# Kernel tuning notes

Hardware: AMD Instinct MI355X
Metric: run time of the kernel (lower is better)

The kernel has to match this reference:

```python
import jax, jax.numpy as jnp
import numpy as np

IMG_SIZE = 224
PATCH_SIZE = 16
CONTEXT_LEN = 316
LATENT_DIM = 1024
NUM_HEADS = 16
NUM_PATCHES = (IMG_SIZE // PATCH_SIZE) ** 2  # 196
SEQ_LEN = NUM_PATCHES + CONTEXT_LEN          # 512
BATCH = 8


def prefix_lm_mask(num_img_patches, total):
    # lower-triangular causal mask, but the image-patch block is fully bidirectional
    m = np.tril(np.ones((total, total), dtype=np.float32))
    m[:num_img_patches, :num_img_patches] = 1.0
    return jnp.asarray(m)  # [S, S], 1 = attend, 0 = masked


def setup_inputs() -> dict:
    key = jax.random.key(0)
    k_x, k_q, k_k, k_v, k_o, k_b = jax.random.split(key, 6)
    d = LATENT_DIM
    scale = 1.0 / np.sqrt(d)
    return {
        "x": jax.random.normal(k_x, (BATCH, SEQ_LEN, d), dtype=jnp.float32),
        "w_q": jax.random.normal(k_q, (d, d), dtype=jnp.float32) * scale,
        "w_k": jax.random.normal(k_k, (d, d), dtype=jnp.float32) * scale,
        "w_v": jax.random.normal(k_v, (d, d), dtype=jnp.float32) * scale,
        "w_o": jax.random.normal(k_o, (d, d), dtype=jnp.float32) * scale,
        "b_o": jax.random.normal(k_b, (d,), dtype=jnp.float32) * 0.01,
    }


def reference(x, w_q, w_k, w_v, w_o, b_o):
    B, S, D = x.shape
    H = NUM_HEADS
    hd = D // H
    # projections (nn.Linear: y = x @ W^T)
    q = (x @ w_q.T).reshape(B, S, H, hd).transpose(0, 2, 1, 3)  # [B,H,S,hd]
    k = (x @ w_k.T).reshape(B, S, H, hd).transpose(0, 2, 1, 3)
    v = (x @ w_v.T).reshape(B, S, H, hd).transpose(0, 2, 1, 3)
    scores = jnp.einsum("bhqd,bhkd->bhqk", q, k) / jnp.sqrt(jnp.float32(hd))
    mask = prefix_lm_mask(NUM_PATCHES, S)  # [S,S]
    scores = jnp.where(mask == 0, jnp.float32(-jnp.inf), scores)
    attn = jax.nn.softmax(scores, axis=-1)
    ctx = jnp.einsum("bhqk,bhkd->bhqd", attn, v)
    ctx = ctx.transpose(0, 2, 1, 3).reshape(B, S, D)
    return ctx @ w_o.T + b_o
```

## Files before the change

kernel.cpp:

```cpp
#include <hip/hip_runtime.h>
#include <stdint.h>
#include <math.h>

#define NB_B 8
#define NB_S 512
#define NB_D 1024
#define NB_H 16
#define NB_HD 64
#define NP 196
#define MTOT 4096

#define OFF_XB 0
#define OFF_WQ 4194304
#define OFF_WK 5242880
#define OFF_WV 6291456
#define OFF_WO 7340032
#define OFF_Q  8388608
#define OFF_K  12582912
#define OFF_VT 16777216
#define OFF_CT 20971520

typedef __attribute__((ext_vector_type(8))) short bf16x8;
typedef __attribute__((ext_vector_type(4))) float f32x4;
typedef __attribute__((ext_vector_type(4))) short s16x4;
typedef __attribute__((ext_vector_type(8))) short s16x8;

__device__ __forceinline__ short f2bf(float f) {
  union { float f; uint32_t u; } c; c.f = f;
  uint32_t r = (c.u + 0x7fffu + ((c.u >> 16) & 1u)) >> 16;
  return (short)r;
}

__device__ __forceinline__ uint32_t pack2bf(float lo, float hi) {
  uint32_t ulo = __float_as_uint(lo) + 0x8000u;
  uint32_t uhi = __float_as_uint(hi) + 0x8000u;
  return __builtin_amdgcn_perm(uhi, ulo, 0x07060302u);
}

__device__ __forceinline__ void async16(void* lds, const void* g) {
  __builtin_amdgcn_global_load_lds(
      (const __attribute__((address_space(1))) void*)g,
      (__attribute__((address_space(3))) void*)lds, 16, 0, 0);
}

__global__ __launch_bounds__(256) void cvt5(const float* __restrict__ x,
                                            const float* __restrict__ wq,
                                            const float* __restrict__ wk,
                                            const float* __restrict__ wv,
                                            const float* __restrict__ wo,
                                            short* __restrict__ ws) {
  __shared__ uint32_t lt[16 * 513];
  int b = blockIdx.x, t = threadIdx.x;
  const float* src; short* dst; float scale;
  if (b < 256) {
    src = x + b * 16384;
    dst = ws + OFF_XB + b * 16384;
    scale = 1.0f;
  } else {
    int wi = (b - 256) >> 6, gn = (b - 256) & 63;
    switch (wi) {
      case 0:  src = wq + gn * 16384; scale = 0.125f; break;
      case 1:  src = wk + gn * 16384; scale = 1.0f;   break;
      case 2:  src = wv + gn * 16384; scale = 1.0f;   break;
      default: src = wo + gn * 16384; scale = 1.0f;   break;
    }
    dst = ws + OFF_WQ + wi * 1048576 + gn * 16384;
  }
#pragma unroll
  for (int i = 0; i < 16; ++i) {
    int flat = t + i * 256;
    int row = flat >> 8, col4 = flat & 255;
    float4 v = *(const float4*)(src + flat * 4);
    uint32_t lo = (uint32_t)(uint16_t)f2bf(v.x * scale) |
                  ((uint32_t)(uint16_t)f2bf(v.y * scale) << 16);
    uint32_t hi = (uint32_t)(uint16_t)f2bf(v.z * scale) |
                  ((uint32_t)(uint16_t)f2bf(v.w * scale) << 16);
    lt[row * 513 + col4 * 2]     = lo;
    lt[row * 513 + col4 * 2 + 1] = hi;
  }
  __syncthreads();
#pragma unroll
  for (int i = 0; i < 8; ++i) {
    int s = t + i * 256;
    int kb = s >> 6, l = s & 63, quad = l >> 4, cc = l & 15;
    int base = cc * 513 + kb * 16 + quad * 4;
    union { uint32_t u[4]; s16x8 v; } o;
    o.u[0] = lt[base];     o.u[1] = lt[base + 1];
    o.u[2] = lt[base + 2]; o.u[3] = lt[base + 3];
    *(s16x8*)(dst + s * 8) = o.v;
  }
}

__global__ __launch_bounds__(256, 2) void gemm_qkv(short* __restrict__ ws) {
  __shared__ __align__(16) short As[4096];
  __shared__ __align__(16) short Bs[4096];
  int bx = blockIdx.x;
  int wsel = bx >> 8;
  int tile = bx & 255;
  int mt = tile >> 3, nt = tile & 7;
  int m0 = mt << 7, n0 = nt << 7;
  const short* A  = ws + OFF_XB;
  const short* Bw = ws + OFF_WQ + wsel * 1048576;
  int t = threadIdx.x, lane = t & 63, wvi = t >> 6;
  int c = lane & 15, quad = lane >> 4;
  int wm = wvi >> 1, wn = wvi & 1;
  int g0 = mt << 3, gn0 = nt << 3;
  f32x4 acc[4][4] = {};

  for (int kk = 0; kk < 1024; kk += 32) {
    int kb = kk >> 5;
#pragma unroll
    for (int i = 0; i < 2; ++i) {
      int ch = wvi * 2 + i;
      async16(&As[ch << 9], A  + ((g0  + ch) * 32 + kb) * 512 + lane * 8);
      async16(&Bs[ch << 9], Bw + ((gn0 + ch) * 32 + kb) * 512 + lane * 8);
    }
    __syncthreads();
    bf16x8 af[4], bfr[4];
#pragma unroll
    for (int i = 0; i < 4; ++i) af[i]  = *(const bf16x8*)&As[((wm * 4 + i) << 9) + lane * 8];
#pragma unroll
    for (int j = 0; j < 4; ++j) bfr[j] = *(const bf16x8*)&Bs[((wn * 4 + j) << 9) + lane * 8];
#pragma unroll
    for (int i = 0; i < 4; ++i)
#pragma unroll
      for (int j = 0; j < 4; ++j)
        acc[i][j] = __builtin_amdgcn_mfma_f32_16x16x32_bf16(af[i], bfr[j], acc[i][j], 0, 0, 0);
    __syncthreads();
  }

#pragma unroll
  for (int i = 0; i < 4; ++i) {
#pragma unroll
    for (int j = 0; j < 4; ++j) {
      int n = n0 + wn * 64 + j * 16 + c;
      int h = n >> 6, d = n & 63;
      int mq = m0 + wm * 64 + i * 16 + quad * 4;
      int bb = mq >> 9, srow = mq & 511;
      if (wsel < 2) {
        int dblk = d >> 5, qk = (d >> 3) & 3, jd = d & 7;
        int g = srow >> 4;
        short* outp = ws + (wsel == 0 ? OFF_Q : OFF_K);
        size_t base = (size_t)(bb * 16 + h) * 32768 +
                      (size_t)(((g * 2 + dblk) * 64 + qk * 16 + quad * 4)) * 8 + jd;
#pragma unroll
        for (int r = 0; r < 4; ++r) outp[base + r * 8] = f2bf(acc[i][j][r]);
      } else {
        int dg = d >> 4, cv = d & 15;
        int kblk = srow >> 5, qv = (srow >> 3) & 3, jv = srow & 7;
        s16x4 o;
#pragma unroll
        for (int r = 0; r < 4; ++r) o[r] = f2bf(acc[i][j][r]);
        *(s16x4*)&ws[OFF_VT + (size_t)(bb * 16 + h) * 32768 +
                     (size_t)((dg * 16 + kblk) * 64 + qv * 16 + cv) * 8 + jv] = o;
      }
    }
  }
}

__global__ __launch_bounds__(256, 2) void attn(short* __restrict__ ws) {
  __shared__ __align__(16) short Kb[8192];
  __shared__ __align__(16) short Vb[8192];
  int bi = blockIdx.x;
  int bh = bi >> 2, qcr = bi & 3;
  int qc = (qcr + bh + 2 * (bh >> 6)) & 3;
  int t = threadIdx.x, lane = t & 63, wvi = t >> 6;
  int c = lane & 15, quad = lane >> 4;
  const short* Qsw  = ws + OFF_Q  + (size_t)bh * 32768;
  const short* Ksw  = ws + OFF_K  + (size_t)bh * 32768;
  const short* Vsw  = ws + OFF_VT + (size_t)bh * 32768;
  short* ct = ws + OFF_CT;
  int b = bh >> 4, h = bh & 15;

  int qt0 = qc * 128 + wvi * 32;
  int qt1 = qt0 + 16;
  int kn0 = (qt0 + 16 > NP) ? (qt0 + 16) : NP;
  int kn1 = (qt1 + 16 > NP) ? (qt1 + 16) : NP;
  int knb = (qc * 128 + 128 > NP) ? (qc * 128 + 128) : NP;
  int NCH = (knb + 127) >> 7;

  int qg0 = qt0 >> 4, qg1 = qt1 >> 4;
  bf16x8 q00 = *(const bf16x8*)(Qsw + ((qg0 * 2 + 0) * 64 + lane) * 8);
  bf16x8 q01 = *(const bf16x8*)(Qsw + ((qg0 * 2 + 1) * 64 + lane) * 8);
  bf16x8 q10 = *(const bf16x8*)(Qsw + ((qg1 * 2 + 0) * 64 + lane) * 8);
  bf16x8 q11 = *(const bf16x8*)(Qsw + ((qg1 * 2 + 1) * 64 + lane) * 8);

  f32x4 acc0[4] = {}, acc1[4] = {};
  float l0 = 0.0f, l1 = 0.0f;
  int L0 = c + ((quad & 1) << 5);
  bool hilo = quad >= 2;

  for (int chn = 0; chn < NCH; ++chn) {
    int k0 = chn << 7;
    {
      int kg0 = k0 >> 4;
      int kblk0 = k0 >> 5;
#pragma unroll
      for (int i = 0; i < 4; ++i) {
        int ch = wvi * 4 + i;
        int kgrel = ch >> 1, f = ch & 1;
        async16(&Kb[ch << 9], Ksw + (((kg0 + kgrel) * 2 + f) * 64 + lane) * 8);
        int dg = ch >> 2, kbrel = ch & 3;
        async16(&Vb[ch << 9], Vsw + ((dg * 16 + kblk0 + kbrel) * 64 + lane) * 8);
      }
    }
    __syncthreads();

#pragma unroll
    for (int hf = 0; hf < 2; ++hf) {
      int kh = k0 + (hf << 6);
      bf16x8 ak[4][2], av[4][2];
#pragma unroll
      for (int mb = 0; mb < 4; ++mb)
#pragma unroll
        for (int f = 0; f < 2; ++f) {
          ak[mb][f] = *(const bf16x8*)&Kb[((((hf * 4 + mb) << 1) + f) << 9) + lane * 8];
          av[mb][f] = *(const bf16x8*)&Vb[(((mb << 2) + (hf << 1) + f) << 9) + lane * 8];
        }

#pragma unroll
      for (int s = 0; s < 2; ++s) {
        int qt = s ? qt1 : qt0;
        int kn = s ? kn1 : kn0;
        if (kh >= kn) continue;
        bf16x8 bq0 = s ? q10 : q00;
        bf16x8 bq1 = s ? q11 : q01;
        f32x4* acc = s ? acc1 : acc0;

        float p[4][4];
#pragma unroll
        for (int mb = 0; mb < 4; ++mb) {
          f32x4 st = {};
          st = __builtin_amdgcn_mfma_f32_16x16x32_bf16(ak[mb][0], bq0, st, 0, 0, 0);
          st = __builtin_amdgcn_mfma_f32_16x16x32_bf16(ak[mb][1], bq1, st, 0, 0, 0);
#pragma unroll
          for (int r = 0; r < 4; ++r) p[mb][r] = __expf(st[r]);
        }

        if ((kh + 64 > NP) && (kh + 64 > qt + 1)) {
          int row = qt + c;
#pragma unroll
          for (int mb = 0; mb < 4; ++mb)
#pragma unroll
            for (int r = 0; r < 4; ++r) {
              int key = kh + mb * 16 + (quad << 2) + r;
              bool v = (row < NP) ? (key < NP) : (key <= row);
              p[mb][r] = v ? p[mb][r] : 0.0f;
            }
        }
        float ls = 0.0f;
#pragma unroll
        for (int mb = 0; mb < 4; ++mb)
#pragma unroll
          for (int r = 0; r < 4; ++r) ls += p[mb][r];
        if (s) l1 += ls; else l0 += ls;

#pragma unroll
        for (int hh = 0; hh < 2; ++hh) {
          float* pa = p[2 * hh];
          float* pb = p[2 * hh + 1];
          uint32_t e0 = pack2bf(pa[0], pa[1]);
          uint32_t e1 = pack2bf(pa[2], pa[3]);
          uint32_t e2 = pack2bf(pb[0], pb[1]);
          uint32_t e3 = pack2bf(pb[2], pb[3]);
          uint32_t a0 = (uint32_t)__shfl((int)e0, L0);
          uint32_t b0 = (uint32_t)__shfl((int)e1, L0);
          uint32_t a1 = (uint32_t)__shfl((int)e0, L0 + 16);
          uint32_t b1 = (uint32_t)__shfl((int)e1, L0 + 16);
          uint32_t c0 = (uint32_t)__shfl((int)e2, L0);
          uint32_t d0 = (uint32_t)__shfl((int)e3, L0);
          uint32_t c1 = (uint32_t)__shfl((int)e2, L0 + 16);
          uint32_t d1 = (uint32_t)__shfl((int)e3, L0 + 16);
          union { uint32_t u[4]; bf16x8 v; } bp;
          bp.u[0] = hilo ? c0 : a0;
          bp.u[1] = hilo ? d0 : b0;
          bp.u[2] = hilo ? c1 : a1;
          bp.u[3] = hilo ? d1 : b1;
#pragma unroll
          for (int db = 0; db < 4; ++db)
            acc[db] = __builtin_amdgcn_mfma_f32_16x16x32_bf16(av[db][hh], bp.v, acc[db], 0, 0, 0);
        }
      }
    }
    __syncthreads();
  }

#pragma unroll
  for (int s = 0; s < 2; ++s) {
    float l = s ? l1 : l0;
    f32x4* acc = s ? acc1 : acc0;
    int qt = s ? qt1 : qt0;
    l += __shfl_xor(l, 16);
    l += __shfl_xor(l, 32);
    float inv = 1.0f / l;
    int g = (b * 512 + qt) >> 4;
#pragma unroll
    for (int db = 0; db < 4; ++db) {
      int col0 = h * 64 + db * 16 + quad * 4;
      int kb = col0 >> 5, qp = (col0 & 31) >> 3, jo = col0 & 7;
      s16x4 o;
#pragma unroll
      for (int r = 0; r < 4; ++r) o[r] = f2bf(acc[db][r] * inv);
      *(s16x4*)&ct[(size_t)((g * 32 + kb) * 64 + qp * 16 + c) * 8 + jo] = o;
    }
  }
}

__global__ __launch_bounds__(256, 2) void gemm_out(const short* __restrict__ ws,
                                                   const float* __restrict__ bias,
                                                   float* __restrict__ out) {
  __shared__ __align__(16) short As[4096];
  __shared__ __align__(16) short Bs[8192];
  int bx = blockIdx.x;
  int mt = bx >> 3, nt = bx & 7;
  int m0 = mt << 6, n0 = nt << 7;
  const short* A  = ws + OFF_CT;
  const short* Bw = ws + OFF_WO;
  int t = threadIdx.x, lane = t & 63, wvi = t >> 6;
  int c = lane & 15, quad = lane >> 4;
  int wm = wvi >> 1, wn = wvi & 1;
  int g0 = m0 >> 4, gn0 = n0 >> 4;
  f32x4 acc[2][4] = {};

  for (int kk = 0; kk < 1024; kk += 64) {
    int kb = kk >> 5;
#pragma unroll
    for (int i = 0; i < 6; ++i) {
      int ch = wvi * 6 + i;
      if (ch < 8) {
        int mg = ch >> 1, kh = ch & 1;
        async16(&As[ch << 9], A + ((g0 + mg) * 32 + kb + kh) * 512 + lane * 8);
      } else {
        int cb = ch - 8, mg = cb >> 1, kh = cb & 1;
        async16(&Bs[cb << 9], Bw + ((gn0 + mg) * 32 + kb + kh) * 512 + lane * 8);
      }
    }
    __syncthreads();

    bf16x8 af[2][2], bfr[4][2];
#pragma unroll
    for (int i = 0; i < 2; ++i)
#pragma unroll
      for (int kh = 0; kh < 2; ++kh)
        af[i][kh] = *(const bf16x8*)&As[((((wm * 2 + i) << 1) + kh) << 9) + lane * 8];
#pragma unroll
    for (int j = 0; j < 4; ++j)
#pragma unroll
      for (int kh = 0; kh < 2; ++kh)
        bfr[j][kh] = *(const bf16x8*)&Bs[((((wn * 4 + j) << 1) + kh) << 9) + lane * 8];
#pragma unroll
    for (int kh = 0; kh < 2; ++kh)
#pragma unroll
      for (int i = 0; i < 2; ++i)
#pragma unroll
        for (int j = 0; j < 4; ++j)
          acc[i][j] = __builtin_amdgcn_mfma_f32_16x16x32_bf16(af[i][kh], bfr[j][kh], acc[i][j], 0, 0, 0);
    __syncthreads();
  }

#pragma unroll
  for (int j = 0; j < 4; ++j) {
    int n = n0 + wn * 64 + j * 16 + c;
    float bj = bias[n];
#pragma unroll
    for (int i = 0; i < 2; ++i) {
      int mq = m0 + wm * 32 + i * 16 + quad * 4;
#pragma unroll
      for (int r = 0; r < 4; ++r)
        out[(size_t)(mq + r) * 1024 + n] = acc[i][j][r] + bj;
    }
  }
}

extern "C" void kernel_launch(void* const* d_in, const int* in_sizes, int n_in,
                              void* d_out, int out_size, void* d_ws, size_t ws_size,
                              hipStream_t stream) {
  (void)in_sizes; (void)n_in; (void)out_size; (void)ws_size;
  const float* x  = (const float*)d_in[0];
  const float* wq = (const float*)d_in[1];
  const float* wk = (const float*)d_in[2];
  const float* wv = (const float*)d_in[3];
  const float* wo = (const float*)d_in[4];
  const float* bo = (const float*)d_in[5];
  short* ws = (short*)d_ws;
  float* out = (float*)d_out;

  cvt5<<<512, 256, 0, stream>>>(x, wq, wk, wv, wo, ws);
  gemm_qkv<<<768, 256, 0, stream>>>(ws);
  attn<<<512, 256, 0, stream>>>(ws);
  gemm_out<<<512, 256, 0, stream>>>(ws, bo, out);
}
```

Baseline: 151.7 us.

## Rewrite QKV GEMM with 256x256 tiles and double-buffered async LDS pipeline

Replaces the 128x128-tile QKV projection GEMM (768 blocks of 256 threads, load-sync-compute per k step) with a 256x256-tile kernel using 512 threads, 192 blocks and a 64-k double-buffered LDS pipeline. Global-to-LDS async loads for the next k step are issued between MFMA phases, with partial vmcnt waits, raw barriers and setprio so memory traffic overlaps compute and per-FLOP operand reuse rises. The risk is that 192 blocks underfill the GPU's compute units, and the 128 KB of LDS per block limits occupancy.

```diff
diff --git a/kernel.cpp b/kernel.cpp
--- a/kernel.cpp
+++ b/kernel.cpp
@@ -91,51 +91,104 @@
   }
 }
 
-__global__ __launch_bounds__(256, 2) void gemm_qkv(short* __restrict__ ws) {
-  __shared__ __align__(16) short As[4096];
-  __shared__ __align__(16) short Bs[4096];
+__global__ __launch_bounds__(512, 2) void gemm_qkv8(short* __restrict__ ws) {
+  __shared__ __align__(16) short LDS[65536];
   int bx = blockIdx.x;
-  int wsel = bx >> 8;
-  int tile = bx & 255;
-  int mt = tile >> 3, nt = tile & 7;
-  int m0 = mt << 7, n0 = nt << 7;
+  int mt = bx / 12, nt = bx % 12;
+  int m0 = mt << 8;
+  int wsel = nt >> 2;
+  int nw0 = (nt & 3) << 8;
   const short* A  = ws + OFF_XB;
-  const short* Bw = ws + OFF_WQ + wsel * 1048576;
-  int t = threadIdx.x, lane = t & 63, wvi = t >> 6;
+  const short* Bw = ws + OFF_WQ;
+  int t0 = threadIdx.x, lane = t0 & 63, wvi = t0 >> 6;
   int c = lane & 15, quad = lane >> 4;
-  int wm = wvi >> 1, wn = wvi & 1;
-  int g0 = mt << 3, gn0 = nt << 3;
-  f32x4 acc[4][4] = {};
-
-  for (int kk = 0; kk < 1024; kk += 32) {
-    int kb = kk >> 5;
-#pragma unroll
-    for (int i = 0; i < 2; ++i) {
-      int ch = wvi * 2 + i;
-      async16(&As[ch << 9], A  + ((g0  + ch) * 32 + kb) * 512 + lane * 8);
-      async16(&Bs[ch << 9], Bw + ((gn0 + ch) * 32 + kb) * 512 + lane * 8);
-    }
-    __syncthreads();
-    bf16x8 af[4], bfr[4];
-#pragma unroll
-    for (int i = 0; i < 4; ++i) af[i]  = *(const bf16x8*)&As[((wm * 4 + i) << 9) + lane * 8];
-#pragma unroll
-    for (int j = 0; j < 4; ++j) bfr[j] = *(const bf16x8*)&Bs[((wn * 4 + j) << 9) + lane * 8];
-#pragma unroll
-    for (int i = 0; i < 4; ++i)
-#pragma unroll
-      for (int j = 0; j < 4; ++j)
-        acc[i][j] = __builtin_amdgcn_mfma_f32_16x16x32_bf16(af[i], bfr[j], acc[i][j], 0, 0, 0);
-    __syncthreads();
-  }
-
-#pragma unroll
-  for (int i = 0; i < 4; ++i) {
+  int wm = wvi >> 2, wn = wvi & 3;
+  f32x4 acc[8][4] = {};
+
+#pragma unroll
+  for (int kkh = 0; kkh < 2; ++kkh) {
+#pragma unroll
+    for (int i2 = 0; i2 < 2; ++i2) {
+      int g = wvi * 2 + i2;
+      async16(&LDS[(g * 2 + kkh) << 9],
+              A + (((mt * 16 + g) * 32 + kkh) << 9) + lane * 8);
+    }
+#pragma unroll
+    for (int i2 = 0; i2 < 2; ++i2) {
+      int g = wvi * 2 + i2;
+      async16(&LDS[32768 + ((g * 2 + kkh) << 9)],
+              Bw + (((nt * 16 + g) * 32 + kkh) << 9) + lane * 8);
+    }
+  }
+  asm volatile("s_waitcnt vmcnt(4)" ::: "memory");
+  __builtin_amdgcn_s_barrier();
+
+  for (int t = 0; t < 16; ++t) {
+    int p = t & 1;
+    short* Ab = &LDS[p << 14];
+    short* Bb = &LDS[32768 + (p << 14)];
+    short* An = &LDS[(p ^ 1) << 14];
+    short* Bn = &LDS[32768 + ((p ^ 1) << 14)];
+    bool st = (t < 15);
+    int kbn = (t + 1) * 2;
+    bf16x8 af[8];
+#pragma unroll
+    for (int kkh = 0; kkh < 2; ++kkh) {
+#pragma unroll
+      for (int nh = 0; nh < 2; ++nh) {
+        bf16x8 bfr[2];
+        if (nh == 0) {
+#pragma unroll
+          for (int i = 0; i < 8; ++i)
+            af[i] = *(const bf16x8*)&Ab[(((wm * 8 + i) * 2 + kkh) << 9) + lane * 8];
+        }
+#pragma unroll
+        for (int j2 = 0; j2 < 2; ++j2)
+          bfr[j2] = *(const bf16x8*)&Bb[(((wn * 4 + nh * 2 + j2) * 2 + kkh) << 9) + lane * 8];
+        if (st) {
+          if (nh == 0) {
+#pragma unroll
+            for (int i2 = 0; i2 < 2; ++i2) {
+              int g = wvi * 2 + i2;
+              async16(&An[(g * 2 + kkh) << 9],
+                      A + (((mt * 16 + g) * 32 + kbn + kkh) << 9) + lane * 8);
+            }
+          } else {
+#pragma unroll
+            for (int i2 = 0; i2 < 2; ++i2) {
+              int g = wvi * 2 + i2;
+              async16(&Bn[(g * 2 + kkh) << 9],
+                      Bw + (((nt * 16 + g) * 32 + kbn + kkh) << 9) + lane * 8);
+            }
+          }
+        }
+        __builtin_amdgcn_s_barrier();
+        asm volatile("s_waitcnt lgkmcnt(0)" ::: "memory");
+        __builtin_amdgcn_sched_barrier(0);
+        __builtin_amdgcn_s_setprio(1);
+#pragma unroll
+        for (int i = 0; i < 8; ++i)
+#pragma unroll
+          for (int j2 = 0; j2 < 2; ++j2)
+            acc[i][nh * 2 + j2] = __builtin_amdgcn_mfma_f32_16x16x32_bf16(
+                af[i], bfr[j2], acc[i][nh * 2 + j2], 0, 0, 0);
+        __builtin_amdgcn_s_setprio(0);
+        if (nh == 1) {
+          if (st) asm volatile("s_waitcnt vmcnt(4)" ::: "memory");
+          else    asm volatile("s_waitcnt vmcnt(0)" ::: "memory");
+        }
+        __builtin_amdgcn_s_barrier();
+      }
+    }
+  }
+
+#pragma unroll
+  for (int i = 0; i < 8; ++i) {
 #pragma unroll
     for (int j = 0; j < 4; ++j) {
-      int n = n0 + wn * 64 + j * 16 + c;
-      int h = n >> 6, d = n & 63;
-      int mq = m0 + wm * 64 + i * 16 + quad * 4;
+      int nf = nw0 + wn * 64 + j * 16 + c;
+      int h = nf >> 6, d = nf & 63;
+      int mq = m0 + wm * 128 + i * 16 + quad * 4;
       int bb = mq >> 9, srow = mq & 511;
       if (wsel < 2) {
         int dblk = d >> 5, qk = (d >> 3) & 3, jd = d & 7;
@@ -386,7 +439,7 @@
   float* out = (float*)d_out;
 
   cvt5<<<512, 256, 0, stream>>>(x, wq, wk, wv, wo, ws);
-  gemm_qkv<<<768, 256, 0, stream>>>(ws);
+  gemm_qkv8<<<192, 512, 0, stream>>>(ws);
   attn<<<512, 256, 0, stream>>>(ws);
   gemm_out<<<512, 256, 0, stream>>>(ws, bo, out);
 }
```

Result: slower. 158.8 us (+4.7%).

## Rewrite QKV GEMM as 128x384 tile with 4-stage async LDS pipeline

Applied to the files above, without the earlier changes.

The QKV projection now runs as 256 blocks of 512 threads, each computing a 128x384 output tile that spans the fused Q/K/V weight matrix. A 4-slot ring of LDS buffers prefetches three k-steps ahead, with split loads interleaved between two MFMA halves, explicit vmcnt waits and s_setprio raised around the MFMA sections. The goal is to hide global-load latency and reuse each A tile across more columns, at the cost of 128KB of LDS per block and fewer blocks than there are CUs.

```diff
diff --git a/kernel.cpp b/kernel.cpp
--- a/kernel.cpp
+++ b/kernel.cpp
@@ -91,51 +91,91 @@
   }
 }
 
-__global__ __launch_bounds__(256, 2) void gemm_qkv(short* __restrict__ ws) {
-  __shared__ __align__(16) short As[4096];
-  __shared__ __align__(16) short Bs[4096];
-  int bx = blockIdx.x;
-  int wsel = bx >> 8;
-  int tile = bx & 255;
-  int mt = tile >> 3, nt = tile & 7;
-  int m0 = mt << 7, n0 = nt << 7;
+__global__ __launch_bounds__(512, 2) void gemm_qkv8(short* __restrict__ ws) {
+  __shared__ __align__(16) short LDS[65536];
+  int bid = blockIdx.x;
+  int mt = bid >> 3, nt = bid & 7;
   const short* A  = ws + OFF_XB;
-  const short* Bw = ws + OFF_WQ + wsel * 1048576;
-  int t = threadIdx.x, lane = t & 63, wvi = t >> 6;
+  const short* Bw = ws + OFF_WQ;
+  int t0 = threadIdx.x, lane = t0 & 63, wvi = t0 >> 6;
   int c = lane & 15, quad = lane >> 4;
-  int wm = wvi >> 1, wn = wvi & 1;
-  int g0 = mt << 3, gn0 = nt << 3;
-  f32x4 acc[4][4] = {};
-
-  for (int kk = 0; kk < 1024; kk += 32) {
-    int kb = kk >> 5;
-#pragma unroll
-    for (int i = 0; i < 2; ++i) {
-      int ch = wvi * 2 + i;
-      async16(&As[ch << 9], A  + ((g0  + ch) * 32 + kb) * 512 + lane * 8);
-      async16(&Bs[ch << 9], Bw + ((gn0 + ch) * 32 + kb) * 512 + lane * 8);
-    }
-    __syncthreads();
-    bf16x8 af[4], bfr[4];
-#pragma unroll
-    for (int i = 0; i < 4; ++i) af[i]  = *(const bf16x8*)&As[((wm * 4 + i) << 9) + lane * 8];
-#pragma unroll
-    for (int j = 0; j < 4; ++j) bfr[j] = *(const bf16x8*)&Bs[((wn * 4 + j) << 9) + lane * 8];
+  int wm = wvi >> 2, wn = wvi & 3;
+  f32x4 acc[4][6] = {};
+
+  int gA  = mt * 8 + wvi;
+  int gB0 = nt * 24 + wvi * 3;
+
+#pragma unroll
+  for (int hs = 0; hs < 3; ++hs) {
+    short* slot = &LDS[hs << 14];
+    async16(&slot[wvi << 9],               A  + ((gA * 32 + hs) << 9) + lane * 8);
+    async16(&slot[(8 + wvi * 3 + 0) << 9], Bw + (((gB0 + 0) * 32 + hs) << 9) + lane * 8);
+    async16(&slot[(8 + wvi * 3 + 1) << 9], Bw + (((gB0 + 1) * 32 + hs) << 9) + lane * 8);
+    async16(&slot[(8 + wvi * 3 + 2) << 9], Bw + (((gB0 + 2) * 32 + hs) << 9) + lane * 8);
+  }
+  asm volatile("s_waitcnt vmcnt(8)" ::: "memory");
+  __builtin_amdgcn_s_barrier();
+
+#pragma unroll 4
+  for (int hh = 0; hh < 32; ++hh) {
+    short* slot = &LDS[(hh & 3) << 14];
+    short* sst  = &LDS[((hh + 3) & 3) << 14];
+    bool st = (hh < 29);
+    int hs = hh + 3;
+    bf16x8 af[4], bfr[3];
 #pragma unroll
     for (int i = 0; i < 4; ++i)
-#pragma unroll
-      for (int j = 0; j < 4; ++j)
+      af[i] = *(const bf16x8*)&slot[((wm * 4 + i) << 9) + lane * 8];
+#pragma unroll
+    for (int j = 0; j < 3; ++j)
+      bfr[j] = *(const bf16x8*)&slot[((8 + wn * 6 + j) << 9) + lane * 8];
+    if (st) {
+      async16(&sst[wvi << 9],               A  + ((gA * 32 + hs) << 9) + lane * 8);
+      async16(&sst[(8 + wvi * 3 + 0) << 9], Bw + ((gB0 * 32 + hs) << 9) + lane * 8);
+    }
+    __builtin_amdgcn_s_barrier();
+    asm volatile("s_waitcnt lgkmcnt(0)" ::: "memory");
+    __builtin_amdgcn_sched_barrier(0);
+    __builtin_amdgcn_s_setprio(1);
+#pragma unroll
+    for (int i = 0; i < 4; ++i)
+#pragma unroll
+      for (int j = 0; j < 3; ++j)
         acc[i][j] = __builtin_amdgcn_mfma_f32_16x16x32_bf16(af[i], bfr[j], acc[i][j], 0, 0, 0);
-    __syncthreads();
+    __builtin_amdgcn_s_setprio(0);
+    __builtin_amdgcn_s_barrier();
+#pragma unroll
+    for (int j = 0; j < 3; ++j)
+      bfr[j] = *(const bf16x8*)&slot[((8 + wn * 6 + 3 + j) << 9) + lane * 8];
+    if (st) {
+      async16(&sst[(8 + wvi * 3 + 1) << 9], Bw + (((gB0 + 1) * 32 + hs) << 9) + lane * 8);
+      async16(&sst[(8 + wvi * 3 + 2) << 9], Bw + (((gB0 + 2) * 32 + hs) << 9) + lane * 8);
+    }
+    __builtin_amdgcn_s_barrier();
+    asm volatile("s_waitcnt lgkmcnt(0)" ::: "memory");
+    __builtin_amdgcn_sched_barrier(0);
+    __builtin_amdgcn_s_setprio(1);
+#pragma unroll
+    for (int i = 0; i < 4; ++i)
+#pragma unroll
+      for (int j = 0; j < 3; ++j)
+        acc[i][3 + j] = __builtin_amdgcn_mfma_f32_16x16x32_bf16(af[i], bfr[j], acc[i][3 + j], 0, 0, 0);
+    __builtin_amdgcn_s_setprio(0);
+    if (hh < 29)       asm volatile("s_waitcnt vmcnt(8)" ::: "memory");
+    else if (hh == 29) asm volatile("s_waitcnt vmcnt(4)" ::: "memory");
+    else               asm volatile("s_waitcnt vmcnt(0)" ::: "memory");
+    __builtin_amdgcn_s_barrier();
   }
 
 #pragma unroll
   for (int i = 0; i < 4; ++i) {
 #pragma unroll
-    for (int j = 0; j < 4; ++j) {
-      int n = n0 + wn * 64 + j * 16 + c;
+    for (int j = 0; j < 6; ++j) {
+      int nf = nt * 384 + wn * 96 + j * 16 + c;
+      int wsel = nf >> 10;
+      int n = nf & 1023;
       int h = n >> 6, d = n & 63;
-      int mq = m0 + wm * 64 + i * 16 + quad * 4;
+      int mq = (mt << 7) + wm * 64 + i * 16 + quad * 4;
       int bb = mq >> 9, srow = mq & 511;
       if (wsel < 2) {
         int dblk = d >> 5, qk = (d >> 3) & 3, jd = d & 7;
@@ -386,7 +426,7 @@
   float* out = (float*)d_out;
 
   cvt5<<<512, 256, 0, stream>>>(x, wq, wk, wv, wo, ws);
-  gemm_qkv<<<768, 256, 0, stream>>>(ws);
+  gemm_qkv8<<<256, 512, 0, stream>>>(ws);
   attn<<<512, 256, 0, stream>>>(ws);
   gemm_out<<<512, 256, 0, stream>>>(ws, bo, out);
 }
```

Result: slower. 155.1 us (+2.2%).

## Load K/V fragments directly from global memory in attention, dropping LDS staging

Applied to the files above, without the earlier changes.

The attention kernel no longer stages 128-key chunks of K and V into shared memory with async copies and block barriers. Each wave now reads its K/V MFMA fragments straight from global memory (L2/cache) in 64-key steps, and stops at its own causal limit instead of the block-wide one. This removes the __syncthreads stalls, the LDS traffic and the shared-memory footprint, and lets waves with short causal ranges finish early. In exchange, the four waves of a block each fetch the same K/V data from global memory, adding redundant cache traffic, and the explicit occupancy hint in launch_bounds is dropped.

```diff
diff --git a/kernel.cpp b/kernel.cpp
--- a/kernel.cpp
+++ b/kernel.cpp
@@ -158,9 +158,7 @@
   }
 }
 
-__global__ __launch_bounds__(256, 2) void attn(short* __restrict__ ws) {
-  __shared__ __align__(16) short Kb[8192];
-  __shared__ __align__(16) short Vb[8192];
+__global__ __launch_bounds__(256) void attn(short* __restrict__ ws) {
   int bi = blockIdx.x;
   int bh = bi >> 2, qcr = bi & 3;
   int qc = (qcr + bh + 2 * (bh >> 6)) & 3;
@@ -176,8 +174,6 @@
   int qt1 = qt0 + 16;
   int kn0 = (qt0 + 16 > NP) ? (qt0 + 16) : NP;
   int kn1 = (qt1 + 16 > NP) ? (qt1 + 16) : NP;
-  int knb = (qc * 128 + 128 > NP) ? (qc * 128 + 128) : NP;
-  int NCH = (knb + 127) >> 7;
 
   int qg0 = qt0 >> 4, qg1 = qt1 >> 4;
   bf16x8 q00 = *(const bf16x8*)(Qsw + ((qg0 * 2 + 0) * 64 + lane) * 8);
@@ -190,99 +186,80 @@
   int L0 = c + ((quad & 1) << 5);
   bool hilo = quad >= 2;
 
-  for (int chn = 0; chn < NCH; ++chn) {
-    int k0 = chn << 7;
-    {
-      int kg0 = k0 >> 4;
-      int kblk0 = k0 >> 5;
-#pragma unroll
-      for (int i = 0; i < 4; ++i) {
-        int ch = wvi * 4 + i;
-        int kgrel = ch >> 1, f = ch & 1;
-        async16(&Kb[ch << 9], Ksw + (((kg0 + kgrel) * 2 + f) * 64 + lane) * 8);
-        int dg = ch >> 2, kbrel = ch & 3;
-        async16(&Vb[ch << 9], Vsw + ((dg * 16 + kblk0 + kbrel) * 64 + lane) * 8);
-      }
-    }
-    __syncthreads();
-
-#pragma unroll
-    for (int hf = 0; hf < 2; ++hf) {
-      int kh = k0 + (hf << 6);
-      bf16x8 ak[4][2], av[4][2];
+  for (int kh = 0; kh < kn1; kh += 64) {
+    bf16x8 ak[4][2], av[4][2];
+    int kg = kh >> 4, kblk = kh >> 5;
+#pragma unroll
+    for (int mb = 0; mb < 4; ++mb) {
+      ak[mb][0] = *(const bf16x8*)(Ksw + (((kg + mb) * 2 + 0) * 64 + lane) * 8);
+      ak[mb][1] = *(const bf16x8*)(Ksw + (((kg + mb) * 2 + 1) * 64 + lane) * 8);
+      av[mb][0] = *(const bf16x8*)(Vsw + ((mb * 16 + kblk + 0) * 64 + lane) * 8);
+      av[mb][1] = *(const bf16x8*)(Vsw + ((mb * 16 + kblk + 1) * 64 + lane) * 8);
+    }
+
+#pragma unroll
+    for (int s = 0; s < 2; ++s) {
+      int qt = s ? qt1 : qt0;
+      int kn = s ? kn1 : kn0;
+      if (kh >= kn) continue;
+      bf16x8 bq0 = s ? q10 : q00;
+      bf16x8 bq1 = s ? q11 : q01;
+      f32x4* acc = s ? acc1 : acc0;
+
+      float p[4][4];
+#pragma unroll
+      for (int mb = 0; mb < 4; ++mb) {
+        f32x4 st = {};
+        st = __builtin_amdgcn_mfma_f32_16x16x32_bf16(ak[mb][0], bq0, st, 0, 0, 0);
+        st = __builtin_amdgcn_mfma_f32_16x16x32_bf16(ak[mb][1], bq1, st, 0, 0, 0);
+#pragma unroll
+        for (int r = 0; r < 4; ++r) p[mb][r] = __expf(st[r]);
+      }
+
+      if ((kh + 64 > NP) && (kh + 64 > qt + 1)) {
+        int row = qt + c;
+#pragma unroll
+        for (int mb = 0; mb < 4; ++mb)
+#pragma unroll
+          for (int r = 0; r < 4; ++r) {
+            int key = kh + mb * 16 + (quad << 2) + r;
+            bool v = (row < NP) ? (key < NP) : (key <= row);
+            p[mb][r] = v ? p[mb][r] : 0.0f;
+          }
+      }
+      float ls = 0.0f;
 #pragma unroll
       for (int mb = 0; mb < 4; ++mb)
 #pragma unroll
-        for (int f = 0; f < 2; ++f) {
-          ak[mb][f] = *(const bf16x8*)&Kb[((((hf * 4 + mb) << 1) + f) << 9) + lane * 8];
-          av[mb][f] = *(const bf16x8*)&Vb[(((mb << 2) + (hf << 1) + f) << 9) + lane * 8];
-        }
-
-#pragma unroll
-      for (int s = 0; s < 2; ++s) {
-        int qt = s ? qt1 : qt0;
-        int kn = s ? kn1 : kn0;
-        if (kh >= kn) continue;
-        bf16x8 bq0 = s ? q10 : q00;
-        bf16x8 bq1 = s ? q11 : q01;
-        f32x4* acc = s ? acc1 : acc0;
-
-        float p[4][4];
-#pragma unroll
-        for (int mb = 0; mb < 4; ++mb) {
-          f32x4 st = {};
-          st = __builtin_amdgcn_mfma_f32_16x16x32_bf16(ak[mb][0], bq0, st, 0, 0, 0);
-          st = __builtin_amdgcn_mfma_f32_16x16x32_bf16(ak[mb][1], bq1, st, 0, 0, 0);
-#pragma unroll
-          for (int r = 0; r < 4; ++r) p[mb][r] = __expf(st[r]);
-        }
-
-        if ((kh + 64 > NP) && (kh + 64 > qt + 1)) {
-          int row = qt + c;
-#pragma unroll
-          for (int mb = 0; mb < 4; ++mb)
-#pragma unroll
-            for (int r = 0; r < 4; ++r) {
-              int key = kh + mb * 16 + (quad << 2) + r;
-              bool v = (row < NP) ? (key < NP) : (key <= row);
-              p[mb][r] = v ? p[mb][r] : 0.0f;
-            }
-        }
-        float ls = 0.0f;
-#pragma unroll
-        for (int mb = 0; mb < 4; ++mb)
-#pragma unroll
-          for (int r = 0; r < 4; ++r) ls += p[mb][r];
-        if (s) l1 += ls; else l0 += ls;
-
-#pragma unroll
-        for (int hh = 0; hh < 2; ++hh) {
-          float* pa = p[2 * hh];
-          float* pb = p[2 * hh + 1];
-          uint32_t e0 = pack2bf(pa[0], pa[1]);
-          uint32_t e1 = pack2bf(pa[2], pa[3]);
-          uint32_t e2 = pack2bf(pb[0], pb[1]);
-          uint32_t e3 = pack2bf(pb[2], pb[3]);
-          uint32_t a0 = (uint32_t)__shfl((int)e0, L0);
-          uint32_t b0 = (uint32_t)__shfl((int)e1, L0);
-          uint32_t a1 = (uint32_t)__shfl((int)e0, L0 + 16);
-          uint32_t b1 = (uint32_t)__shfl((int)e1, L0 + 16);
-          uint32_t c0 = (uint32_t)__shfl((int)e2, L0);
-          uint32_t d0 = (uint32_t)__shfl((int)e3, L0);
-          uint32_t c1 = (uint32_t)__shfl((int)e2, L0 + 16);
-          uint32_t d1 = (uint32_t)__shfl((int)e3, L0 + 16);
-          union { uint32_t u[4]; bf16x8 v; } bp;
-          bp.u[0] = hilo ? c0 : a0;
-          bp.u[1] = hilo ? d0 : b0;
-          bp.u[2] = hilo ? c1 : a1;
-          bp.u[3] = hilo ? d1 : b1;
-#pragma unroll
-          for (int db = 0; db < 4; ++db)
-            acc[db] = __builtin_amdgcn_mfma_f32_16x16x32_bf16(av[db][hh], bp.v, acc[db], 0, 0, 0);
-        }
-      }
-    }
-    __syncthreads();
+        for (int r = 0; r < 4; ++r) ls += p[mb][r];
+      if (s) l1 += ls; else l0 += ls;
+
+#pragma unroll
+      for (int hh = 0; hh < 2; ++hh) {
+        float* pa = p[2 * hh];
+        float* pb = p[2 * hh + 1];
+        uint32_t e0 = pack2bf(pa[0], pa[1]);
+        uint32_t e1 = pack2bf(pa[2], pa[3]);
+        uint32_t e2 = pack2bf(pb[0], pb[1]);
+        uint32_t e3 = pack2bf(pb[2], pb[3]);
+        uint32_t a0 = (uint32_t)__shfl((int)e0, L0);
+        uint32_t b0 = (uint32_t)__shfl((int)e1, L0);
+        uint32_t a1 = (uint32_t)__shfl((int)e0, L0 + 16);
+        uint32_t b1 = (uint32_t)__shfl((int)e1, L0 + 16);
+        uint32_t c0 = (uint32_t)__shfl((int)e2, L0);
+        uint32_t d0 = (uint32_t)__shfl((int)e3, L0);
+        uint32_t c1 = (uint32_t)__shfl((int)e2, L0 + 16);
+        uint32_t d1 = (uint32_t)__shfl((int)e3, L0 + 16);
+        union { uint32_t u[4]; bf16x8 v; } bp;
+        bp.u[0] = hilo ? c0 : a0;
+        bp.u[1] = hilo ? d0 : b0;
+        bp.u[2] = hilo ? c1 : a1;
+        bp.u[3] = hilo ? d1 : b1;
+#pragma unroll
+        for (int db = 0; db < 4; ++db)
+          acc[db] = __builtin_amdgcn_mfma_f32_16x16x32_bf16(av[db][hh], bp.v, acc[db], 0, 0, 0);
+      }
+    }
   }
 
 #pragma unroll
```

Result: no change. 153.6 us (+1.2%).
